# Kernel optimization log

Hardware: AMD Instinct MI355X
Metric: run time of the kernel (lower is better)

## Reference

```python
import jax, jax.numpy as jnp
import numpy as np

EPS = 1e-5
C = 64  # in_channels == feat_channels == out_channels


def _ln(x, g, b):
    m = jnp.mean(x, axis=-1, keepdims=True)
    v = jnp.mean(jnp.square(x - m), axis=-1, keepdims=True)
    return (x - m) * jax.lax.rsqrt(v + EPS) * g + b


def setup_inputs() -> dict:
    key = jax.random.key(0)
    ks = jax.random.split(key, 10)
    bs, nc, H, W = 8, 80, 256, 256
    d = {
        "feat": jax.random.normal(ks[0], (bs, C, H, W), jnp.float32),
        "head": jax.random.normal(ks[1], (bs, nc, C, 1), jnp.float32),
        "pred": jax.random.normal(ks[2], (bs, nc, H // 2, W // 2), jnp.float32),
        # linear transforms (stored [in, out], applied as x @ W + b)
        "W_pred_t": jax.random.normal(ks[3], (C, 2 * C), jnp.float32) * 0.05,
        "b_pred_t": jnp.zeros((2 * C,), jnp.float32),
        "W_head_t": jax.random.normal(ks[4], (C, 2 * C), jnp.float32) * 0.05,
        "b_head_t": jnp.zeros((2 * C,), jnp.float32),
        "W_pred_g": jax.random.normal(ks[5], (C, C), jnp.float32) * 0.05,
        "b_pred_g": jnp.zeros((C,), jnp.float32),
        "W_head_g": jax.random.normal(ks[6], (C, C), jnp.float32) * 0.05,
        "b_head_g": jnp.zeros((C,), jnp.float32),
        "W_fc": jax.random.normal(ks[7], (C, C), jnp.float32) * 0.05,
        "b_fc": jnp.zeros((C,), jnp.float32),
        # layernorm params
        "g_pin": jnp.ones((C,), jnp.float32), "be_pin": jnp.zeros((C,), jnp.float32),
        "g_hin": jnp.ones((C,), jnp.float32), "be_hin": jnp.zeros((C,), jnp.float32),
        "g_pout": jnp.ones((C,), jnp.float32), "be_pout": jnp.zeros((C,), jnp.float32),
        "g_hout": jnp.ones((C,), jnp.float32), "be_hout": jnp.zeros((C,), jnp.float32),
        "g_fc": jnp.ones((C,), jnp.float32), "be_fc": jnp.zeros((C,), jnp.float32),
    }
    return d


def reference(feat, head, pred,
              W_pred_t, b_pred_t, W_head_t, b_head_t,
              W_pred_g, b_pred_g, W_head_g, b_head_g,
              W_fc, b_fc,
              g_pin, be_pin, g_hin, be_hin,
              g_pout, be_pout, g_hout, be_hout,
              g_fc, be_fc):
    bs, nc = head.shape[:2]
    H, W = feat.shape[2], feat.shape[3]
    pred_up = jax.image.resize(pred, (bs, nc, H, W), method="bilinear")
    pred_up = jax.nn.sigmoid(pred_up)
    # head-aware feature assembly: [bs, nc, C]
    assemble = jnp.einsum("bnhw,bchw->bnc", pred_up, feat)
    a = assemble.reshape(-1, C)                      # [BN, C]
    BN = a.shape[0]
    # head: [bs, nc, C, kk] -> [BN, kk, C]
    hd = jnp.transpose(head.reshape(bs, nc, C, -1), (0, 1, 3, 2)).reshape(BN, -1, C)

    pf = a @ W_pred_t + b_pred_t                     # [BN, 2C]
    pf_in, pf_out = pf[:, :C], pf[:, C:]
    hf = hd @ W_head_t + b_head_t                    # [BN, kk, 2C]
    hf_in, hf_out = hf[..., :C], hf[..., C:]

    gate = hf_in * pf_in[:, None, :]                 # [BN, kk, C]
    head_gate = jax.nn.sigmoid(_ln(gate @ W_head_g + b_head_g, g_hin, be_hin))
    pred_gate = jax.nn.sigmoid(_ln(gate @ W_pred_g + b_pred_g, g_pin, be_pin))

    hf_out = _ln(hf_out, g_hout, be_hout)
    pf_out = _ln(pf_out, g_pout, be_pout)

    upd = pred_gate * pf_out[:, None, :] + head_gate * hf_out
    upd = jax.nn.relu(_ln(upd @ W_fc + b_fc, g_fc, be_fc))
    upd = upd.reshape(bs, nc, -1, C)
    upd = jnp.transpose(upd, (0, 1, 3, 2)).reshape(bs, nc, C, 1, 1)
    return upd
```

## Files before the change

kernel.cpp:

```cpp
#include <hip/hip_runtime.h>
#include <hip/hip_bf16.h>
#include <hip/hip_fp16.h>


using bf16x8 = __attribute__((ext_vector_type(8))) short;
using f32x4  = __attribute__((ext_vector_type(4))) float;

#define NPART 128
#define ROWS 2

#define LGKM_BARRIER() do { \
  asm volatile("s_waitcnt lgkmcnt(0)" ::: "memory"); \
  __builtin_amdgcn_s_barrier(); } while (0)

__device__ __forceinline__ unsigned pk2(float lo, float hi) {
  union { __hip_bfloat162 h2; unsigned u; } cv;
  cv.h2 = __float22bfloat162_rn(make_float2(lo, hi));
  return cv.u;
}
__device__ __forceinline__ float sigAB(float a, float b) {
  return __builtin_amdgcn_rcpf(1.0f + __builtin_amdgcn_exp2f(-0.36067376f * a - 1.08202128f * b));
}
__device__ __forceinline__ float sigBA(float a, float b) {
  return __builtin_amdgcn_rcpf(1.0f + __builtin_amdgcn_exp2f(-1.08202128f * a - 0.36067376f * b));
}

__global__ __launch_bounds__(256) void k_assemble(
    const float* __restrict__ feat, const float* __restrict__ pred,
    __half* __restrict__ partial) {
  __shared__ __align__(16) unsigned short Pfrag[40 * 64 * 8];

  const int tid = threadIdx.x;
  const int b  = blockIdx.x >> 7;
  const int rb = blockIdx.x & 127;
  const int wid = tid >> 6, l = tid & 63;
  const int ch16 = l & 15, kg = l >> 4;
  const int c0 = wid << 4;
  const int h0 = rb * ROWS;
  const int gg = tid & 31, nb = tid >> 5;

  f32x4 acc[5] = {};
  const float* fwave = feat + (((size_t)(b * 64 + c0 + ch16)) << 16);
  const float* pbat  = pred + (((size_t)(b * 80)) << 14);

  #pragma unroll
  for (int r = 0; r < ROWS; ++r) {
    const int h = h0 + r;
    const int j = h >> 1;
    int r0, r1; float wy0, wy1;
    if ((h & 1) == 0) { r0 = (j > 0) ? j - 1 : 0; r1 = j; wy0 = 0.25f; wy1 = 0.75f; }
    else              { r0 = j; r1 = (j < 127) ? j + 1 : 127; wy0 = 0.75f; wy1 = 0.25f; }

    float y[10][4];
    #pragma unroll
    for (int i = 0; i < 10; ++i) {
      const int n = nb + 8 * i;
      const float* pb = pbat + (((size_t)n) << 14);
      const float4 v0 = *(const float4*)(pb + (r0 << 7) + gg * 4);
      const float4 v1 = *(const float4*)(pb + (r1 << 7) + gg * 4);
      y[i][0] = wy0 * v0.x + wy1 * v1.x; y[i][1] = wy0 * v0.y + wy1 * v1.y;
      y[i][2] = wy0 * v0.z + wy1 * v1.z; y[i][3] = wy0 * v0.w + wy1 * v1.w;
    }

    const float* fb = fwave + h * 256;
    float4 f[16];
    #pragma unroll
    for (int ks = 0; ks < 8; ++ks) {
      const int pw = ks * 32 + kg * 8;
      f[2 * ks]     = *(const float4*)(fb + pw);
      f[2 * ks + 1] = *(const float4*)(fb + pw + 4);
    }

    #pragma unroll
    for (int i = 0; i < 10; ++i) {
      const int n = nb + 8 * i;
      const float y0 = y[i][0], y1 = y[i][1], y2 = y[i][2], y3 = y[i][3];
      float yl = __shfl_up(y3, 1, 64);   if (gg == 0)  yl = y0;
      float yr = __shfl_down(y0, 1, 64); if (gg == 31) yr = y3;
      float P[8];
      P[0] = sigAB(yl, y0); P[1] = sigBA(y0, y1);
      P[2] = sigAB(y0, y1); P[3] = sigBA(y1, y2);
      P[4] = sigAB(y1, y2); P[5] = sigBA(y2, y3);
      P[6] = sigAB(y2, y3); P[7] = sigBA(y3, yr);
      uint4 s;
      s.x = pk2(P[0], P[1]); s.y = pk2(P[2], P[3]);
      s.z = pk2(P[4], P[5]); s.w = pk2(P[6], P[7]);
      const int ks = gg >> 2, kgw = gg & 3;
      const int slot = kgw * 16 + ((n & 15) ^ ks);
      *(uint4*)&Pfrag[(((ks * 5 + (n >> 4)) * 64) + slot) * 8] = s;
    }
    LGKM_BARRIER();

    #pragma unroll
    for (int ks = 0; ks < 8; ++ks) {
      const float4 f0 = f[2 * ks], f1 = f[2 * ks + 1];
      union { uint4 u; bf16x8 v; } bu;
      bu.u.x = pk2(f0.x, f0.y); bu.u.y = pk2(f0.z, f0.w);
      bu.u.z = pk2(f1.x, f1.y); bu.u.w = pk2(f1.z, f1.w);
      const int slot = kg * 16 + (ch16 ^ ks);
      #pragma unroll
      for (int m = 0; m < 5; ++m) {
        const bf16x8 af = *(const bf16x8*)&Pfrag[(((ks * 5 + m) * 64) + slot) * 8];
        acc[m] = __builtin_amdgcn_mfma_f32_16x16x32_bf16(af, bu.v, acc[m], 0, 0, 0);
      }
    }
    LGKM_BARRIER();
  }

  __half* po = partial + ((size_t)(b * NPART + rb)) * (80 * 64);
  #pragma unroll
  for (int m = 0; m < 5; ++m) {
    #pragma unroll
    for (int q = 0; q < 4; ++q) {
      const int n = m * 16 + kg * 4 + q;
      po[n * 64 + c0 + ch16] = __float2half(acc[m][q]);
    }
  }
}

__device__ __forceinline__ float wred64(float v) {
  #pragma unroll
  for (int off = 32; off > 0; off >>= 1) v += __shfl_xor(v, off, 64);
  return v;
}
__device__ __forceinline__ float lnorm(float x, const float* __restrict__ g,
                                       const float* __restrict__ be, int l) {
  const float m = wred64(x) * 0.015625f;
  const float d = x - m;
  const float var = wred64(d * d) * 0.015625f;
  return d * rsqrtf(var + 1e-5f) * g[l] + be[l];
}
__device__ __forceinline__ float sigmf(float x) {
  return __builtin_amdgcn_rcpf(1.0f + __builtin_amdgcn_exp2f(-1.44269504f * x));
}

__global__ __launch_bounds__(256) void k_head(
    const __half* __restrict__ partial, const float* __restrict__ head,
    const float* __restrict__ Wpt, const float* __restrict__ bpt,
    const float* __restrict__ Wht, const float* __restrict__ bht,
    const float* __restrict__ Wpg, const float* __restrict__ bpg,
    const float* __restrict__ Whg, const float* __restrict__ bhg,
    const float* __restrict__ Wfc, const float* __restrict__ bfc,
    const float* __restrict__ g_pin, const float* __restrict__ be_pin,
    const float* __restrict__ g_hin, const float* __restrict__ be_hin,
    const float* __restrict__ g_pout, const float* __restrict__ be_pout,
    const float* __restrict__ g_hout, const float* __restrict__ be_hout,
    const float* __restrict__ g_fc, const float* __restrict__ be_fc,
    float* __restrict__ out, int npart) {
  __shared__ float red[4][64];
  __shared__ float buf[4][64];
  const int tid = threadIdx.x, c = tid & 63, q = tid >> 6;
  const int r = blockIdx.x;
  const int b = r / 80, n = r % 80;
  const int npq = npart >> 2;

  const __half* pp = partial + ((size_t)b * npart + (size_t)q * npq) * 5120 + n * 64 + c;
  float s = 0.f;
  #pragma unroll 8
  for (int jj = 0; jj < npq; ++jj) s += __half2float(pp[(size_t)jj * 5120]);
  red[q][c] = s;
  __syncthreads();

  if (q == 0) {
    const float a_c = red[0][c] + red[1][c] + red[2][c] + red[3][c];
    buf[0][c] = a_c;
    buf[1][c] = head[(size_t)r * 64 + c];

    float pf_in = bpt[c], pf_out = bpt[64 + c];
    float hf_in = bht[c], hf_out = bht[64 + c];
    #pragma unroll 8
    for (int k = 0; k < 64; ++k) {
      const float av = buf[0][k];
      const float hv = buf[1][k];
      pf_in  += av * Wpt[k * 128 + c];
      pf_out += av * Wpt[k * 128 + 64 + c];
      hf_in  += hv * Wht[k * 128 + c];
      hf_out += hv * Wht[k * 128 + 64 + c];
    }
    buf[2][c] = hf_in * pf_in;

    float hg = bhg[c], pg = bpg[c];
    #pragma unroll 8
    for (int k = 0; k < 64; ++k) {
      const float gv = buf[2][k];
      hg += gv * Whg[k * 64 + c];
      pg += gv * Wpg[k * 64 + c];
    }
    const float head_gate = sigmf(lnorm(hg, g_hin, be_hin, c));
    const float pred_gate = sigmf(lnorm(pg, g_pin, be_pin, c));
    const float hfo = lnorm(hf_out, g_hout, be_hout, c);
    const float pfo = lnorm(pf_out, g_pout, be_pout, c);
    buf[3][c] = pred_gate * pfo + head_gate * hfo;

    float fc = bfc[c];
    #pragma unroll 8
    for (int k = 0; k < 64; ++k)
      fc += buf[3][k] * Wfc[k * 64 + c];
    float o = lnorm(fc, g_fc, be_fc, c);
    out[(size_t)r * 64 + c] = fmaxf(o, 0.f);
  }
}

extern "C" void kernel_launch(void* const* d_in, const int* in_sizes, int n_in,
                              void* d_out, int out_size, void* d_ws, size_t ws_size,
                              hipStream_t stream) {
  const float* feat   = (const float*)d_in[0];
  const float* head   = (const float*)d_in[1];
  const float* pred   = (const float*)d_in[2];
  const float* Wpt    = (const float*)d_in[3];
  const float* bpt    = (const float*)d_in[4];
  const float* Wht    = (const float*)d_in[5];
  const float* bht    = (const float*)d_in[6];
  const float* Wpg    = (const float*)d_in[7];
  const float* bpg    = (const float*)d_in[8];
  const float* Whg    = (const float*)d_in[9];
  const float* bhg    = (const float*)d_in[10];
  const float* Wfc    = (const float*)d_in[11];
  const float* bfc    = (const float*)d_in[12];
  const float* g_pin  = (const float*)d_in[13];
  const float* be_pin = (const float*)d_in[14];
  const float* g_hin  = (const float*)d_in[15];
  const float* be_hin = (const float*)d_in[16];
  const float* g_pout = (const float*)d_in[17];
  const float* be_pout= (const float*)d_in[18];
  const float* g_hout = (const float*)d_in[19];
  const float* be_hout= (const float*)d_in[20];
  const float* g_fc   = (const float*)d_in[21];
  const float* be_fc  = (const float*)d_in[22];
  float* out = (float*)d_out;
  __half* partial = (__half*)d_ws;

  hipLaunchKernelGGL(k_assemble, dim3(8 * NPART), dim3(256), 0, stream,
                     feat, pred, partial);
  hipLaunchKernelGGL(k_head, dim3(640), dim3(256), 0, stream,
                     partial, head, Wpt, bpt, Wht, bht, Wpg, bpg, Whg, bhg,
                     Wfc, bfc, g_pin, be_pin, g_hin, be_hin, g_pout, be_pout,
                     g_hout, be_hout, g_fc, be_fc, out, NPART);
}
```

Before: 63.07 us.

## Restructure assemble kernel into 4-row half-width tiles reusing pred rows

Each block now handles four output rows over half the width instead of two full rows, with a block-index swizzle across batches. Source pred rows are loaded once and reused across adjacent output rows through register rotation, and the next row's pred loads are issued before the MFMA phase of the current row. The LDS fragment buffer is halved, the swizzle includes an extra XOR term, and launch bounds request higher occupancy. The cost is more barriers per block and extra edge-column scalar loads.

New measurement: 58.99 us. 6.5% less time.

```diff
diff --git a/kernel.cpp b/kernel.cpp
--- a/kernel.cpp
+++ b/kernel.cpp
@@ -5,13 +5,6 @@
 
 using bf16x8 = __attribute__((ext_vector_type(8))) short;
 using f32x4  = __attribute__((ext_vector_type(4))) float;
-
-#define NPART 128
-#define ROWS 2
-
-#define LGKM_BARRIER() do { \
-  asm volatile("s_waitcnt lgkmcnt(0)" ::: "memory"); \
-  __builtin_amdgcn_s_barrier(); } while (0)
 
 __device__ __forceinline__ unsigned pk2(float lo, float hi) {
   union { __hip_bfloat162 h2; unsigned u; } cv;
@@ -25,95 +18,133 @@
   return __builtin_amdgcn_rcpf(1.0f + __builtin_amdgcn_exp2f(-1.08202128f * a - 0.36067376f * b));
 }
 
-__global__ __launch_bounds__(256) void k_assemble(
+__device__ __forceinline__ void produce_row(
+    const float4 (&pL)[5], const float4 (&pH)[5],
+    const float (&sL)[5], const float (&sH)[5],
+    int half, int gg, int nbp, unsigned short* __restrict__ Pfrag) {
+  #pragma unroll
+  for (int i = 0; i < 5; ++i) {
+    const float sc = 0.25f * sL[i] + 0.75f * sH[i];
+    const float y0 = 0.25f * pL[i].x + 0.75f * pH[i].x;
+    const float y1 = 0.25f * pL[i].y + 0.75f * pH[i].y;
+    const float y2 = 0.25f * pL[i].z + 0.75f * pH[i].z;
+    const float y3 = 0.25f * pL[i].w + 0.75f * pH[i].w;
+    float yl = __shfl_up(y3, 1, 16);
+    float yr = __shfl_down(y0, 1, 16);
+    if (gg == 0)  yl = half ? sc : y0;
+    if (gg == 15) yr = half ? y3 : sc;
+    float P[8];
+    P[0] = sigAB(yl, y0); P[1] = sigBA(y0, y1);
+    P[2] = sigAB(y0, y1); P[3] = sigBA(y1, y2);
+    P[4] = sigAB(y1, y2); P[5] = sigBA(y2, y3);
+    P[6] = sigAB(y2, y3); P[7] = sigBA(y3, yr);
+    uint4 s;
+    s.x = pk2(P[0], P[1]); s.y = pk2(P[2], P[3]);
+    s.z = pk2(P[4], P[5]); s.w = pk2(P[6], P[7]);
+    const int ks = gg >> 2, kgw = gg & 3;
+    const int slot = kgw * 16 + ((nbp ^ ks ^ (kgw << 1)) & 15);
+    *(uint4*)&Pfrag[(((ks * 5 + i) * 64) + slot) * 8] = s;
+  }
+}
+
+__device__ __forceinline__ void mfma_row(
+    const float* __restrict__ fb, const unsigned short* __restrict__ Pfrag,
+    int ch16, int kg, f32x4 (&acc)[5]) {
+  #pragma unroll
+  for (int ks = 0; ks < 4; ++ks) {
+    const int pw = ks * 32 + kg * 8;
+    const float4 f0 = *(const float4*)(fb + pw);
+    const float4 f1 = *(const float4*)(fb + pw + 4);
+    union { uint4 u; bf16x8 v; } bu;
+    bu.u.x = pk2(f0.x, f0.y); bu.u.y = pk2(f0.z, f0.w);
+    bu.u.z = pk2(f1.x, f1.y); bu.u.w = pk2(f1.z, f1.w);
+    const int slot = kg * 16 + ((ch16 ^ ks ^ (kg << 1)) & 15);
+    #pragma unroll
+    for (int m = 0; m < 5; ++m) {
+      const bf16x8 af = *(const bf16x8*)&Pfrag[(((ks * 5 + m) * 64) + slot) * 8];
+      acc[m] = __builtin_amdgcn_mfma_f32_16x16x32_bf16(af, bu.v, acc[m], 0, 0, 0);
+    }
+  }
+}
+
+__global__ __launch_bounds__(256, 4) void k_assemble_quad(
     const float* __restrict__ feat, const float* __restrict__ pred,
     __half* __restrict__ partial) {
-  __shared__ __align__(16) unsigned short Pfrag[40 * 64 * 8];
+  __shared__ __align__(16) unsigned short Pfrag[20 * 64 * 8];
+
+  const int bid = blockIdx.x;
+  const int wg  = (bid & 7) * 128 + (bid >> 3);
+  const int half = wg & 1;
+  const int q    = (wg >> 1) & 63;
+  const int b    = wg >> 7;
 
   const int tid = threadIdx.x;
-  const int b  = blockIdx.x >> 7;
-  const int rb = blockIdx.x & 127;
+  const int gg = tid & 15, nbp = tid >> 4;
   const int wid = tid >> 6, l = tid & 63;
-  const int ch16 = l & 15, kg = l >> 4;
-  const int c0 = wid << 4;
-  const int h0 = rb * ROWS;
-  const int gg = tid & 31, nb = tid >> 5;
+  const int ch16 = l & 15, kg = l >> 4, c0 = wid << 4;
+
+  const int rA = (q > 0) ? 2 * q - 1 : 0;
+  const int rB = 2 * q;
+  const int rC = 2 * q + 1;
+  const int rD = (q < 63) ? 2 * q + 2 : 127;
+
+  const int cbase = half << 6;
+  const int csc   = 64 - half;
+  const float* pbat  = pred + (((size_t)(b * 80)) << 14);
+  const float* fbase = feat + (((size_t)(b * 64 + c0 + ch16)) << 16) + (half << 7);
+  const int h0 = 4 * q;
 
   f32x4 acc[5] = {};
-  const float* fwave = feat + (((size_t)(b * 64 + c0 + ch16)) << 16);
-  const float* pbat  = pred + (((size_t)(b * 80)) << 14);
-
-  #pragma unroll
-  for (int r = 0; r < ROWS; ++r) {
-    const int h = h0 + r;
-    const int j = h >> 1;
-    int r0, r1; float wy0, wy1;
-    if ((h & 1) == 0) { r0 = (j > 0) ? j - 1 : 0; r1 = j; wy0 = 0.25f; wy1 = 0.75f; }
-    else              { r0 = j; r1 = (j < 127) ? j + 1 : 127; wy0 = 0.75f; wy1 = 0.25f; }
-
-    float y[10][4];
-    #pragma unroll
-    for (int i = 0; i < 10; ++i) {
-      const int n = nb + 8 * i;
-      const float* pb = pbat + (((size_t)n) << 14);
-      const float4 v0 = *(const float4*)(pb + (r0 << 7) + gg * 4);
-      const float4 v1 = *(const float4*)(pb + (r1 << 7) + gg * 4);
-      y[i][0] = wy0 * v0.x + wy1 * v1.x; y[i][1] = wy0 * v0.y + wy1 * v1.y;
-      y[i][2] = wy0 * v0.z + wy1 * v1.z; y[i][3] = wy0 * v0.w + wy1 * v1.w;
-    }
-
-    const float* fb = fwave + h * 256;
-    float4 f[16];
-    #pragma unroll
-    for (int ks = 0; ks < 8; ++ks) {
-      const int pw = ks * 32 + kg * 8;
-      f[2 * ks]     = *(const float4*)(fb + pw);
-      f[2 * ks + 1] = *(const float4*)(fb + pw + 4);
-    }
-
-    #pragma unroll
-    for (int i = 0; i < 10; ++i) {
-      const int n = nb + 8 * i;
-      const float y0 = y[i][0], y1 = y[i][1], y2 = y[i][2], y3 = y[i][3];
-      float yl = __shfl_up(y3, 1, 64);   if (gg == 0)  yl = y0;
-      float yr = __shfl_down(y0, 1, 64); if (gg == 31) yr = y3;
-      float P[8];
-      P[0] = sigAB(yl, y0); P[1] = sigBA(y0, y1);
-      P[2] = sigAB(y0, y1); P[3] = sigBA(y1, y2);
-      P[4] = sigAB(y1, y2); P[5] = sigBA(y2, y3);
-      P[6] = sigAB(y2, y3); P[7] = sigBA(y3, yr);
-      uint4 s;
-      s.x = pk2(P[0], P[1]); s.y = pk2(P[2], P[3]);
-      s.z = pk2(P[4], P[5]); s.w = pk2(P[6], P[7]);
-      const int ks = gg >> 2, kgw = gg & 3;
-      const int slot = kgw * 16 + ((n & 15) ^ ks);
-      *(uint4*)&Pfrag[(((ks * 5 + (n >> 4)) * 64) + slot) * 8] = s;
-    }
-    LGKM_BARRIER();
-
-    #pragma unroll
-    for (int ks = 0; ks < 8; ++ks) {
-      const float4 f0 = f[2 * ks], f1 = f[2 * ks + 1];
-      union { uint4 u; bf16x8 v; } bu;
-      bu.u.x = pk2(f0.x, f0.y); bu.u.y = pk2(f0.z, f0.w);
-      bu.u.z = pk2(f1.x, f1.y); bu.u.w = pk2(f1.z, f1.w);
-      const int slot = kg * 16 + (ch16 ^ ks);
-      #pragma unroll
-      for (int m = 0; m < 5; ++m) {
-        const bf16x8 af = *(const bf16x8*)&Pfrag[(((ks * 5 + m) * 64) + slot) * 8];
-        acc[m] = __builtin_amdgcn_mfma_f32_16x16x32_bf16(af, bu.v, acc[m], 0, 0, 0);
-      }
-    }
-    LGKM_BARRIER();
-  }
-
-  __half* po = partial + ((size_t)(b * NPART + rb)) * (80 * 64);
+  float4 pU[5], pV[5];
+  float sU[5], sV[5];
+
+  #pragma unroll
+  for (int i = 0; i < 5; ++i) {
+    const float* pb = pbat + (((size_t)(nbp + 16 * i)) << 14);
+    pU[i] = *(const float4*)(pb + (rA << 7) + cbase + 4 * gg);
+    pV[i] = *(const float4*)(pb + (rB << 7) + cbase + 4 * gg);
+    sU[i] = pb[(rA << 7) + csc];
+    sV[i] = pb[(rB << 7) + csc];
+  }
+
+  produce_row(pU, pV, sU, sV, half, gg, nbp, Pfrag);
+  __syncthreads();
+  #pragma unroll
+  for (int i = 0; i < 5; ++i) {
+    const float* pb = pbat + (((size_t)(nbp + 16 * i)) << 14);
+    pU[i] = *(const float4*)(pb + (rC << 7) + cbase + 4 * gg);
+    sU[i] = pb[(rC << 7) + csc];
+  }
+  mfma_row(fbase + (size_t)(h0 + 0) * 256, Pfrag, ch16, kg, acc);
+  __syncthreads();
+
+  produce_row(pU, pV, sU, sV, half, gg, nbp, Pfrag);
+  __syncthreads();
+  mfma_row(fbase + (size_t)(h0 + 1) * 256, Pfrag, ch16, kg, acc);
+  __syncthreads();
+
+  produce_row(pV, pU, sV, sU, half, gg, nbp, Pfrag);
+  __syncthreads();
+  #pragma unroll
+  for (int i = 0; i < 5; ++i) {
+    const float* pb = pbat + (((size_t)(nbp + 16 * i)) << 14);
+    pV[i] = *(const float4*)(pb + (rD << 7) + cbase + 4 * gg);
+    sV[i] = pb[(rD << 7) + csc];
+  }
+  mfma_row(fbase + (size_t)(h0 + 2) * 256, Pfrag, ch16, kg, acc);
+  __syncthreads();
+
+  produce_row(pV, pU, sV, sU, half, gg, nbp, Pfrag);
+  __syncthreads();
+  mfma_row(fbase + (size_t)(h0 + 3) * 256, Pfrag, ch16, kg, acc);
+
+  __half* po = partial + ((size_t)(b * 128 + q * 2 + half)) * (80 * 64);
   #pragma unroll
   for (int m = 0; m < 5; ++m) {
     #pragma unroll
-    for (int q = 0; q < 4; ++q) {
-      const int n = m * 16 + kg * 4 + q;
-      po[n * 64 + c0 + ch16] = __float2half(acc[m][q]);
+    for (int qq = 0; qq < 4; ++qq) {
+      const int n = m * 16 + kg * 4 + qq;
+      po[n * 64 + c0 + ch16] = __float2half(acc[m][qq]);
     }
   }
 }
@@ -230,10 +261,10 @@
   float* out = (float*)d_out;
   __half* partial = (__half*)d_ws;
 
-  hipLaunchKernelGGL(k_assemble, dim3(8 * NPART), dim3(256), 0, stream,
+  hipLaunchKernelGGL(k_assemble_quad, dim3(1024), dim3(256), 0, stream,
                      feat, pred, partial);
   hipLaunchKernelGGL(k_head, dim3(640), dim3(256), 0, stream,
                      partial, head, Wpt, bpt, Wht, bht, Wpg, bpg, Whg, bhg,
                      Wfc, bfc, g_pin, be_pin, g_hin, be_hin, g_pout, be_pout,
-                     g_hout, be_hout, g_fc, be_fc, out, NPART);
-}
+                     g_hout, be_hout, g_fc, be_fc, out, 128);
+}
```
